# Kernel tuning notes

Hardware: AMD Instinct MI355X
Metric: run time of the kernel (lower is better)

Reference implementation:

```python
import jax, jax.numpy as jnp
import numpy as np

N, D, H, F, T = 2048, 256, 4, 64, 64
HF = H * F


def setup_inputs() -> dict:
    key = jax.random.key(0)
    ks = jax.random.split(key, 24)
    f32 = jnp.float32
    emb = jax.random.normal(ks[0], (N, D), f32)
    y_as_x = jax.random.normal(ks[1], (N, T), f32)
    adj = (jax.random.uniform(ks[2], (N, N)) < 0.02).astype(f32)
    u = lambda k, shape, s: jax.random.uniform(k, shape, f32, -s, s)
    stdv = 1.0 / np.sqrt(HF)
    inp = dict(emb=emb, y_as_x=y_as_x, adj=adj)
    for i, p in enumerate(['pos', 'neg']):
        o = 3 + i * 6
        inp[p + '_w'] = u(ks[o], (D, HF), stdv)
        inp[p + '_wu'] = u(ks[o + 1], (H, F), 1.0)
        inp[p + '_wv'] = u(ks[o + 2], (H, F), 1.0)
        inp[p + '_b'] = u(ks[o + 3], (1, HF), stdv)
        inp[p + '_pw'] = u(ks[o + 4], (D, HF), 0.02)
        inp[p + '_pb'] = jnp.zeros((HF,), f32)
    inp['self_w'] = u(ks[15], (D, D), 0.02)
    inp['self_b'] = jnp.zeros((D,), f32)
    inp['mlp_pos_w'] = u(ks[16], (HF, D), 0.02)
    inp['mlp_pos_b'] = jnp.zeros((D,), f32)
    inp['mlp_neg_w'] = u(ks[17], (HF, D), 0.02)
    inp['mlp_neg_b'] = jnp.zeros((D,), f32)
    inp['sem_w1'] = u(ks[18], (D, D), 0.02)
    inp['sem_b1'] = jnp.zeros((D,), f32)
    inp['sem_w2'] = u(ks[19], (D, 1), 0.02)
    return inp


def _gat(x, mask, w, wu, wv, b, pw, pb):
    # x: [N,D], mask: [N,N] bool; multi-head GAT with dense masked softmax
    s = (x @ w).reshape(N, H, F).transpose(1, 0, 2)          # [H,N,F]
    f1 = jnp.einsum('hnf,hf->hn', s, wu)                     # u-score per node
    f2 = jnp.einsum('hnf,hf->hn', s, wv)                     # v-score per node
    logits = f1[:, None, :] + f2[:, :, None]                 # [H,N,N], i<-j
    logits = jax.nn.leaky_relu(logits, 0.2)
    masked = jnp.where(mask[None], logits, -1e9)
    attn = jnp.where(mask[None], jax.nn.softmax(masked, axis=2), 0.0)
    out = jnp.einsum('hij,hjf->hif', attn, s)                # [H,N,F]
    out = out.transpose(1, 0, 2).reshape(N, HF) + b
    return out + x @ pw + pb


def reference(emb, y_as_x, adj, pos_w, pos_wu, pos_wv, pos_b, pos_pw, pos_pb,
              neg_w, neg_wu, neg_wv, neg_b, neg_pw, neg_pb,
              self_w, self_b, mlp_pos_w, mlp_pos_b, mlp_neg_w, mlp_neg_b,
              sem_w1, sem_b1, sem_w2):
    # batched pairwise correlation (replaces the per-node Python loop)
    yc = y_as_x - y_as_x.mean(axis=1, keepdims=True)         # centered
    dot = yc @ yc.T                                          # [N,N]
    std = jnp.sqrt((yc ** 2).sum(axis=1) / (T - 1))          # torch std: ddof=1
    corr = dot / (std[:, None] * std[None, :])
    edge = adj != 0
    pos_mask = edge & (corr >= 0.1)
    neg_mask = edge & (corr < 0.1)

    pos_sup = _gat(emb, pos_mask, pos_w, pos_wu, pos_wv, pos_b, pos_pw, pos_pb)
    neg_sup = _gat(emb, neg_mask, neg_w, neg_wu, neg_wv, neg_b, neg_pw, neg_pb)

    sup = emb @ self_w + self_b
    pos_sup = pos_sup @ mlp_pos_w + mlp_pos_b
    neg_sup = neg_sup @ mlp_neg_w + mlp_neg_b

    all_emb = jnp.stack((sup, pos_sup, neg_sup), axis=1)     # [N,3,D]
    # semantic attention over the 3 relation channels
    wlog = jnp.tanh(all_emb @ sem_w1 + sem_b1) @ sem_w2      # [N,3,1]
    beta = jax.nn.softmax(wlog, axis=1)
    x = (beta * all_emb).sum(axis=1)                         # [N,D]
    # PairNorm PN-SI
    x = x - x.mean(axis=0)
    rownorm = jnp.sqrt(1e-6 + (x ** 2).sum(axis=1, keepdims=True))
    return x / rownorm
```

## Files before the change

### kernel.cpp

```cpp
#include <hip/hip_runtime.h>
#include <hip/hip_bf16.h>

#define KN  2048
#define KD  256
#define KH  4
#define KF  64
#define KT  64
#define NCS 32

typedef __attribute__((ext_vector_type(8))) short short8;
typedef __attribute__((ext_vector_type(4))) float floatx4;

__device__ __forceinline__ float wave_sum(float v) {
    #pragma unroll
    for (int o = 32; o > 0; o >>= 1) v += __shfl_xor(v, o, 64);
    return v;
}
__device__ __forceinline__ float wave_max(float v) {
    #pragma unroll
    for (int o = 32; o > 0; o >>= 1) v = fmaxf(v, __shfl_xor(v, o, 64));
    return v;
}
__device__ __forceinline__ short f2bs(float x) {
    union { __hip_bfloat16 h; short s; } u;
    u.h = __float2bfloat16(x);
    return u.s;
}

__global__ __launch_bounds__(256) void setup_kernel(const float* __restrict__ y,
                                                    float* __restrict__ ycs) {
    int w = threadIdx.x >> 6, lane = threadIdx.x & 63;
    int n = blockIdx.x * 4 + w;
    float v = y[n * KT + lane];
    float mean = wave_sum(v) * (1.0f / KT);
    float yc = v - mean;
    float ss = wave_sum(yc * yc);
    ycs[n * KT + lane] = yc * rsqrtf(ss * (1.0f / (KT - 1)));
}

__device__ __forceinline__ void corr_body(const float* __restrict__ ycs,
                                          const float* __restrict__ adj,
                                          unsigned char* __restrict__ code,
                                          int blk, char* smem) {
    float (*As)[68] = (float(*)[68])smem;
    float (*Bs)[68] = (float(*)[68])(smem + 4352);
    int bi = 0, rem = blk;
    while (rem >= 32 - bi) { rem -= 32 - bi; bi++; }
    int bj = bi + rem;
    int i0 = bi * 64, j0 = bj * 64;
    int t = threadIdx.x;
    int tx = t & 15, ty = t >> 4;
    int ar = t >> 2, ac = (t & 3) * 4;
    float acc[4][4] = {};
    for (int kt = 0; kt < KT; kt += 16) {
        float4 a4 = *reinterpret_cast<const float4*>(&ycs[(size_t)(i0 + ar) * KT + kt + ac]);
        float4 b4 = *reinterpret_cast<const float4*>(&ycs[(size_t)(j0 + ar) * KT + kt + ac]);
        As[ac + 0][ar] = a4.x; As[ac + 1][ar] = a4.y; As[ac + 2][ar] = a4.z; As[ac + 3][ar] = a4.w;
        Bs[ac + 0][ar] = b4.x; Bs[ac + 1][ar] = b4.y; Bs[ac + 2][ar] = b4.z; Bs[ac + 3][ar] = b4.w;
        __syncthreads();
        #pragma unroll
        for (int kk = 0; kk < 16; kk++) {
            float4 av = *reinterpret_cast<const float4*>(&As[kk][ty * 4]);
            float4 bv = *reinterpret_cast<const float4*>(&Bs[kk][tx * 4]);
            float a4v[4] = {av.x, av.y, av.z, av.w};
            float b4v[4] = {bv.x, bv.y, bv.z, bv.w};
            #pragma unroll
            for (int ii = 0; ii < 4; ii++)
                #pragma unroll
                for (int jj = 0; jj < 4; jj++) acc[ii][jj] += a4v[ii] * b4v[jj];
        }
        __syncthreads();
    }
    #pragma unroll
    for (int ii = 0; ii < 4; ii++) {
        int i = i0 + ty * 4 + ii;
        int jb = j0 + tx * 4;
        float4 av4 = *reinterpret_cast<const float4*>(&adj[(size_t)i * KN + jb]);
        float a4v[4] = {av4.x, av4.y, av4.z, av4.w};
        uchar4 cc;
        unsigned char* c = (unsigned char*)&cc;
        #pragma unroll
        for (int jj = 0; jj < 4; jj++)
            c[jj] = (a4v[jj] != 0.0f) ? ((acc[ii][jj] >= 0.1f) ? 1 : 2) : 0;
        *reinterpret_cast<uchar4*>(&code[(size_t)i * KN + jb]) = cc;
    }
    if (bi != bj) {
        #pragma unroll
        for (int jj = 0; jj < 4; jj++) {
            int j = j0 + tx * 4 + jj;
            int ib = i0 + ty * 4;
            float4 av4 = *reinterpret_cast<const float4*>(&adj[(size_t)j * KN + ib]);
            float a4v[4] = {av4.x, av4.y, av4.z, av4.w};
            uchar4 cc;
            unsigned char* c = (unsigned char*)&cc;
            #pragma unroll
            for (int ii = 0; ii < 4; ii++)
                c[ii] = (a4v[ii] != 0.0f) ? ((acc[ii][jj] >= 0.1f) ? 1 : 2) : 0;
            *reinterpret_cast<uchar4*>(&code[(size_t)j * KN + ib]) = cc;
        }
    }
}

template <bool TANH>
__device__ __forceinline__ void mfma_gemm_body(
    const float* __restrict__ A, int lda, int bm,
    const float* __restrict__ B, int ldb, int bn,
    const float* __restrict__ bias,
    float* __restrict__ C, int ldc, int cn,
    float* __restrict__ f1h, float* __restrict__ f2h,
    const float* __restrict__ wu_h, const float* __restrict__ wv_h,
    char* smem)
{
    short* As = (short*)smem;
    short* Bs = (short*)(smem + 5120);
    int t = threadIdx.x;
    int w = t >> 6, lane = t & 63;
    int m16 = lane & 15, kq = lane >> 4;
    floatx4 acc0 = {0,0,0,0}, acc1 = {0,0,0,0}, acc2 = {0,0,0,0}, acc3 = {0,0,0,0};
    int ar = t >> 2, acq = (t & 3) * 8;
    int bnn = t & 63, bkg = (t >> 6) * 8;
    for (int kt = 0; kt < KD; kt += 32) {
        const float* pa = &A[(size_t)(bm + ar) * lda + kt + acq];
        float4 a0 = *(const float4*)pa;
        float4 a1 = *(const float4*)(pa + 4);
        short8 av;
        av[0] = f2bs(a0.x); av[1] = f2bs(a0.y); av[2] = f2bs(a0.z); av[3] = f2bs(a0.w);
        av[4] = f2bs(a1.x); av[5] = f2bs(a1.y); av[6] = f2bs(a1.z); av[7] = f2bs(a1.w);
        const float* pb = &B[(size_t)(kt + bkg) * ldb + bn + bnn];
        short8 bv;
        #pragma unroll
        for (int u = 0; u < 8; u++) bv[u] = f2bs(pb[(size_t)u * ldb]);
        __syncthreads();
        *(short8*)&As[ar * 40 + acq] = av;
        *(short8*)&Bs[bnn * 40 + bkg] = bv;
        __syncthreads();
        short8 af  = *(short8*)&As[(w * 16 + m16) * 40 + kq * 8];
        short8 bf0 = *(short8*)&Bs[( 0 + m16) * 40 + kq * 8];
        short8 bf1 = *(short8*)&Bs[(16 + m16) * 40 + kq * 8];
        short8 bf2 = *(short8*)&Bs[(32 + m16) * 40 + kq * 8];
        short8 bf3 = *(short8*)&Bs[(48 + m16) * 40 + kq * 8];
        acc0 = __builtin_amdgcn_mfma_f32_16x16x32_bf16(af, bf0, acc0, 0, 0, 0);
        acc1 = __builtin_amdgcn_mfma_f32_16x16x32_bf16(af, bf1, acc1, 0, 0, 0);
        acc2 = __builtin_amdgcn_mfma_f32_16x16x32_bf16(af, bf2, acc2, 0, 0, 0);
        acc3 = __builtin_amdgcn_mfma_f32_16x16x32_bf16(af, bf3, acc3, 0, 0, 0);
    }
    int row0 = bm + w * 16 + kq * 4;
    floatx4 accs[4] = {acc0, acc1, acc2, acc3};
    #pragma unroll
    for (int nb = 0; nb < 4; nb++) {
        #pragma unroll
        for (int r = 0; r < 4; r++) {
            int col = nb * 16 + m16;
            float v = accs[nb][r] + (bias ? bias[col] : 0.0f);
            if (TANH) {
                float vc = fminf(fmaxf(v, -9.0f), 9.0f);
                float ex = __expf(2.0f * vc);
                v = (ex - 1.0f) / (ex + 1.0f);
            }
            C[(size_t)(row0 + r) * ldc + cn + col] = v;
        }
    }
    if (f1h) {
        float wuv[4], wvv[4];
        #pragma unroll
        for (int nb = 0; nb < 4; nb++) { wuv[nb] = wu_h[nb * 16 + m16]; wvv[nb] = wv_h[nb * 16 + m16]; }
        #pragma unroll
        for (int r = 0; r < 4; r++) {
            float p1 = accs[0][r] * wuv[0] + accs[1][r] * wuv[1] + accs[2][r] * wuv[2] + accs[3][r] * wuv[3];
            float p2 = accs[0][r] * wvv[0] + accs[1][r] * wvv[1] + accs[2][r] * wvv[2] + accs[3][r] * wvv[3];
            #pragma unroll
            for (int o = 1; o < 16; o <<= 1) {
                p1 += __shfl_xor(p1, o, 64);
                p2 += __shfl_xor(p2, o, 64);
            }
            if (m16 == 0) { f1h[row0 + r] = p1; f2h[row0 + r] = p2; }
        }
    }
}

struct EmbPtrs {
    float *S_pos, *S_neg, *P_pos, *P_neg, *sup;
    float *f1p, *f2p, *f1n, *f2n;
};
__global__ __launch_bounds__(256, 4) void phase1_kernel(
    const float* __restrict__ ycs, const float* __restrict__ adj,
    unsigned char* __restrict__ code,
    const float* __restrict__ emb,
    const float* __restrict__ pos_w, const float* __restrict__ neg_w,
    const float* __restrict__ pos_pw, const float* __restrict__ neg_pw,
    const float* __restrict__ self_w,
    const float* __restrict__ pos_pb, const float* __restrict__ neg_pb,
    const float* __restrict__ self_b,
    const float* __restrict__ pos_wu, const float* __restrict__ pos_wv,
    const float* __restrict__ neg_wu, const float* __restrict__ neg_wv,
    float* __restrict__ colsum, EmbPtrs ep)
{
    __shared__ alignas(16) char smem[10240];
    int blk = blockIdx.x;
    if (blk < 528) {
        corr_body(ycs, adj, code, blk, smem);
        return;
    }
    if (blk >= 1168) {
        for (int j = threadIdx.x; j < NCS * KD; j += 256) colsum[j] = 0.0f;
        return;
    }
    int b = blk - 528;
    int tn = b % 20, tm = b / 20;
    int buf = tn >> 2, coloff = (tn & 3) * 64;
    int h = tn & 3;
    const float* B; const float* bias; float* C;
    float *f1h = nullptr, *f2h = nullptr;
    const float *wu_h = nullptr, *wv_h = nullptr;
    if (buf == 0) {
        B = pos_w;  bias = nullptr; C = ep.S_pos;
        f1h = ep.f1p + h * KN; f2h = ep.f2p + h * KN;
        wu_h = pos_wu + h * KF; wv_h = pos_wv + h * KF;
    } else if (buf == 1) {
        B = neg_w;  bias = nullptr; C = ep.S_neg;
        f1h = ep.f1n + h * KN; f2h = ep.f2n + h * KN;
        wu_h = neg_wu + h * KF; wv_h = neg_wv + h * KF;
    } else if (buf == 2) { B = pos_pw; bias = pos_pb + coloff;  C = ep.P_pos; }
    else if (buf == 3)   { B = neg_pw; bias = neg_pb + coloff;  C = ep.P_neg; }
    else                 { B = self_w; bias = self_b + coloff;  C = ep.sup; }
    mfma_gemm_body<false>(emb, KD, tm * 64, B, KD, coloff, bias,
                          C, KD, coloff, f1h, f2h, wu_h, wv_h, smem);
}

__global__ __launch_bounds__(256, 4) void gemm_mlp(const float* __restrict__ Astack,
                                                   const float* __restrict__ B0,
                                                   const float* __restrict__ B1,
                                                   const float* __restrict__ b0,
                                                   const float* __restrict__ b1,
                                                   float* __restrict__ Cstack,
                                                   const float* __restrict__ sup,
                                                   const float* __restrict__ semw1,
                                                   const float* __restrict__ semb1,
                                                   float* __restrict__ T0) {
    __shared__ alignas(16) char smem[10240];
    int by = blockIdx.y;
    int cn = blockIdx.x * 64;
    if (by < 64) {
        int bm = by * 64;
        bool sel = bm >= KN;
        mfma_gemm_body<false>(Astack, KD, bm, sel ? B1 : B0, KD, cn,
                              (sel ? b1 : b0) + cn, Cstack, KD, cn,
                              nullptr, nullptr, nullptr, nullptr, smem);
    } else {
        int bm = (by - 64) * 64;
        mfma_gemm_body<true>(sup, KD, bm, semw1, KD, cn,
                             semb1 + cn, T0, KD, cn,
                             nullptr, nullptr, nullptr, nullptr, smem);
    }
}

__global__ __launch_bounds__(256, 4) void gemm_sem(const float* __restrict__ Astack,
                                                   const float* __restrict__ B,
                                                   const float* __restrict__ bias,
                                                   float* __restrict__ Cstack) {
    __shared__ alignas(16) char smem[10240];
    int cn = blockIdx.x * 64;
    mfma_gemm_body<true>(Astack, KD, blockIdx.y * 64, B, KD, cn,
                         bias + cn, Cstack, KD, cn,
                         nullptr, nullptr, nullptr, nullptr, smem);
}

#define MAXE 256
__global__ __launch_bounds__(256) void attn_kernel(
    const unsigned char* __restrict__ code,
    const float* __restrict__ f1p, const float* __restrict__ f2p,
    const float* __restrict__ Sp, const float* __restrict__ Pp,
    const float* __restrict__ bp, float* __restrict__ Gp,
    const float* __restrict__ f1n, const float* __restrict__ f2n,
    const float* __restrict__ Sn, const float* __restrict__ Pn,
    const float* __restrict__ bn_, float* __restrict__ Gn)
{
    __shared__ alignas(16) int jlp[MAXE];
    __shared__ alignas(16) int jln[MAXE];
    __shared__ alignas(16) float lg[2][KH][MAXE];
    __shared__ int cntp, cntn;
    int i = blockIdx.x;
    int w = threadIdx.x >> 6, lane = threadIdx.x & 63;
    if (threadIdx.x == 0) { cntp = 0; cntn = 0; }
    __syncthreads();
    unsigned long long lmask = (1ull << lane) - 1ull;
    #pragma unroll
    for (int it = 0; it < 2; it++) {
        int base = w * 512 + it * 256;
        uchar4 cv = *reinterpret_cast<const uchar4*>(&code[(size_t)i * KN + base + lane * 4]);
        const unsigned char* ce = (const unsigned char*)&cv;
        #pragma unroll
        for (int e = 0; e < 4; e++) {
            bool ip = (ce[e] == (unsigned char)1);
            bool in_ = (ce[e] == (unsigned char)2);
            unsigned long long balp = __ballot(ip);
            unsigned long long baln = __ballot(in_);
            int tp = __popcll(balp), tn = __popcll(baln);
            int basep = 0, basen = 0;
            if (lane == 0) {
                if (tp) basep = atomicAdd(&cntp, tp);
                if (tn) basen = atomicAdd(&cntn, tn);
            }
            basep = __shfl(basep, 0, 64);
            basen = __shfl(basen, 0, 64);
            int j = base + lane * 4 + e;
            if (ip) { int idx = basep + __popcll(balp & lmask); if (idx < MAXE) jlp[idx] = j; }
            if (in_) { int idx = basen + __popcll(baln & lmask); if (idx < MAXE) jln[idx] = j; }
        }
    }
    __syncthreads();
    int cp = cntp; if (cp > MAXE) cp = MAXE;
    int cn2 = cntn; if (cn2 > MAXE) cn2 = MAXE;
    int cpR = (cp + 3) & ~3, cnR = (cn2 + 3) & ~3;
    if (threadIdx.x < cpR - cp) jlp[cp + threadIdx.x] = 0;
    if (threadIdx.x < cnR - cn2) jln[cn2 + threadIdx.x] = 0;
    __syncthreads();
    int h = w;
    int g = lane >> 4, q4 = (lane & 15) * 4;
    #pragma unroll
    for (int rel = 0; rel < 2; rel++) {
        const int* jl = rel ? jln : jlp;
        int count = rel ? cn2 : cp;
        int countR = rel ? cnR : cpR;
        const float* f1 = rel ? f1n : f1p;
        const float* f2 = rel ? f2n : f2p;
        const float* S  = rel ? Sn : Sp;
        const float* P  = rel ? Pn : Pp;
        const float* b  = rel ? bn_ : bp;
        float* G        = rel ? Gn : Gp;
        float* lgr = lg[rel][h];
        float f2i = f2[h * KN + i];
        float m = -1e30f;
        for (int k = lane; k < count; k += 64) {
            float x = f1[h * KN + jl[k]] + f2i;
            x = (x > 0.0f) ? x : 0.2f * x;
            lgr[k] = x;
            m = fmaxf(m, x);
        }
        m = wave_max(m);
        float ps = 0.0f;
        for (int k = lane; k < count; k += 64) {
            float e = __expf(lgr[k] - m);
            lgr[k] = e;
            ps += e;
        }
        float denom = wave_sum(ps);
        for (int k2 = count + lane; k2 < countR; k2 += 64) lgr[k2] = 0.0f;
        const float* Sh4 = S + h * KF + q4;
        float ax = 0.0f, ay = 0.0f, az = 0.0f, aw = 0.0f;
        for (int k = 0; k < countR; k += 4) {
            int j = jl[k + g];
            float wgt = lgr[k + g];
            float4 sv = *reinterpret_cast<const float4*>(&Sh4[(size_t)j * KD]);
            ax += wgt * sv.x; ay += wgt * sv.y; az += wgt * sv.z; aw += wgt * sv.w;
        }
        #pragma unroll
        for (int o = 16; o < 64; o <<= 1) {
            ax += __shfl_xor(ax, o, 64); ay += __shfl_xor(ay, o, 64);
            az += __shfl_xor(az, o, 64); aw += __shfl_xor(aw, o, 64);
        }
        if (g == 0) {
            float inv = count ? (1.0f / denom) : 0.0f;
            int col = h * KF + q4;
            size_t idx = (size_t)i * KD + col;
            float4 pv = *reinterpret_cast<const float4*>(&P[idx]);
            float4 o4;
            o4.x = ax * inv + b[col + 0] + pv.x;
            o4.y = ay * inv + b[col + 1] + pv.y;
            o4.z = az * inv + b[col + 2] + pv.z;
            o4.w = aw * inv + b[col + 3] + pv.w;
            *reinterpret_cast<float4*>(&G[idx]) = o4;
        }
    }
}

__global__ __launch_bounds__(256) void combine_kernel(const float* __restrict__ T0,
                                                      const float* __restrict__ T1,
                                                      const float* __restrict__ T2,
                                                      const float* __restrict__ w2,
                                                      const float* __restrict__ sup,
                                                      const float* __restrict__ psup,
                                                      const float* __restrict__ nsup,
                                                      float* __restrict__ X,
                                                      float* __restrict__ colsum) {
    int n = blockIdx.x, d = threadIdx.x;
    size_t idx = (size_t)n * KD + d;
    float w2d = w2[d];
    float p0 = T0[idx] * w2d, p1 = T1[idx] * w2d, p2 = T2[idx] * w2d;
    __shared__ float sbuf[4][3];
    int wv = d >> 6, lane = d & 63;
    float s0 = wave_sum(p0), s1 = wave_sum(p1), s2 = wave_sum(p2);
    if (lane == 0) { sbuf[wv][0] = s0; sbuf[wv][1] = s1; sbuf[wv][2] = s2; }
    __syncthreads();
    float w0 = sbuf[0][0] + sbuf[1][0] + sbuf[2][0] + sbuf[3][0];
    float w1 = sbuf[0][1] + sbuf[1][1] + sbuf[2][1] + sbuf[3][1];
    float w2l = sbuf[0][2] + sbuf[1][2] + sbuf[2][2] + sbuf[3][2];
    float mm = fmaxf(w0, fmaxf(w1, w2l));
    float e0 = __expf(w0 - mm), e1 = __expf(w1 - mm), e2 = __expf(w2l - mm);
    float inv = 1.0f / (e0 + e1 + e2);
    float x = (e0 * inv) * sup[idx] + (e1 * inv) * psup[idx] + (e2 * inv) * nsup[idx];
    X[idx] = x;
    atomicAdd(&colsum[(n & (NCS - 1)) * KD + d], x);
}

__global__ __launch_bounds__(256) void final_kernel(const float* __restrict__ X,
                                                    const float* __restrict__ colsum,
                                                    float* __restrict__ out) {
    int n = blockIdx.x, d = threadIdx.x;
    float cs = 0.0f;
    #pragma unroll
    for (int r = 0; r < NCS; r++) cs += colsum[r * KD + d];
    float mean = cs * (1.0f / KN);
    float xc = X[(size_t)n * KD + d] - mean;
    __shared__ float sbuf[4];
    int wv = d >> 6, lane = d & 63;
    float s = wave_sum(xc * xc);
    if (lane == 0) sbuf[wv] = s;
    __syncthreads();
    float ss = sbuf[0] + sbuf[1] + sbuf[2] + sbuf[3];
    out[(size_t)n * KD + d] = xc * rsqrtf(1e-6f + ss);
}

extern "C" void kernel_launch(void* const* d_in, const int* in_sizes, int n_in,
                              void* d_out, int out_size, void* d_ws, size_t ws_size,
                              hipStream_t stream) {
    typedef const float* fp;
    fp emb    = (fp)d_in[0];
    fp y_as_x = (fp)d_in[1];
    fp adj    = (fp)d_in[2];
    fp pos_w  = (fp)d_in[3],  pos_wu = (fp)d_in[4],  pos_wv = (fp)d_in[5];
    fp pos_b  = (fp)d_in[6],  pos_pw = (fp)d_in[7],  pos_pb = (fp)d_in[8];
    fp neg_w  = (fp)d_in[9],  neg_wu = (fp)d_in[10], neg_wv = (fp)d_in[11];
    fp neg_b  = (fp)d_in[12], neg_pw = (fp)d_in[13], neg_pb = (fp)d_in[14];
    fp self_w = (fp)d_in[15], self_b = (fp)d_in[16];
    fp mlp_pos_w = (fp)d_in[17], mlp_pos_b = (fp)d_in[18];
    fp mlp_neg_w = (fp)d_in[19], mlp_neg_b = (fp)d_in[20];
    fp sem_w1 = (fp)d_in[21], sem_b1 = (fp)d_in[22], sem_w2 = (fp)d_in[23];
    float* out = (float*)d_out;

    char* ws = (char*)d_ws;
    float* ycs        = (float*)(ws + 0x0000000);
    unsigned char* cd = (unsigned char*)(ws + 0x0080000);
    float* S_pos      = (float*)(ws + 0x0480000);
    float* S_neg      = (float*)(ws + 0x0680000);
    float* P_pos      = (float*)(ws + 0x0880000);
    float* P_neg      = (float*)(ws + 0x0A80000);
    float* G_pos      = (float*)(ws + 0x0C80000);
    float* G_neg      = (float*)(ws + 0x0E80000);
    float* sup        = (float*)(ws + 0x1080000);
    float* psup       = (float*)(ws + 0x1280000);
    float* nsup       = (float*)(ws + 0x1480000);
    float* colsum     = (float*)(ws + 0x1680000);
    float* f1p        = (float*)(ws + 0x1700000);
    float* f2p        = (float*)(ws + 0x1708000);
    float* f1n        = (float*)(ws + 0x1710000);
    float* f2n        = (float*)(ws + 0x1718000);
    float* T0 = P_pos, *T1 = P_neg, *T2 = G_pos, *X = G_neg;

    setup_kernel<<<512, 256, 0, stream>>>(y_as_x, ycs);

    EmbPtrs ep = {S_pos, S_neg, P_pos, P_neg, sup, f1p, f2p, f1n, f2n};
    phase1_kernel<<<528 + 640 + 1, 256, 0, stream>>>(ycs, adj, cd, emb,
                                                     pos_w, neg_w, pos_pw, neg_pw, self_w,
                                                     pos_pb, neg_pb, self_b,
                                                     pos_wu, pos_wv, neg_wu, neg_wv,
                                                     colsum, ep);

    attn_kernel<<<KN, 256, 0, stream>>>(cd,
                                        f1p, f2p, S_pos, P_pos, pos_b, G_pos,
                                        f1n, f2n, S_neg, P_neg, neg_b, G_neg);

    gemm_mlp<<<dim3(4, 96), 256, 0, stream>>>(G_pos, mlp_pos_w, mlp_neg_w,
                                              mlp_pos_b, mlp_neg_b, psup,
                                              sup, sem_w1, sem_b1, T0);
    gemm_sem<<<dim3(4, 64), 256, 0, stream>>>(psup, sem_w1, sem_b1, T1);

    combine_kernel<<<KN, 256, 0, stream>>>(T0, T1, T2, sem_w2, sup, psup, nsup, X, colsum);
    final_kernel<<<KN, 256, 0, stream>>>(X, colsum, out);
}
```

Before: 171.7 us.

## Fuse all stages into one persistent kernel with software grid barriers

Replaces the seven separate kernel launches with a single persistent mega-kernel of 768 blocks. Each former kernel becomes a grid-stride loop over virtual blocks, and stages are separated by atomic-counter grid barriers. The barrier counters are zeroed by a memset before launch. The aim is to remove launch and inter-kernel drain gaps, at the cost of spin-wait barriers, a requirement that all 768 blocks be co-resident, and lower parallelism in stages that previously used more blocks.

After: 648.2 us. +277.6%, slower.

```diff
diff --git a/kernel.cpp b/kernel.cpp
--- a/kernel.cpp
+++ b/kernel.cpp
@@ -7,6 +7,8 @@
 #define KF  64
 #define KT  64
 #define NCS 32
+#define MAXE 256
+#define NBLK 768
 
 typedef __attribute__((ext_vector_type(8))) short short8;
 typedef __attribute__((ext_vector_type(4))) float floatx4;
@@ -27,16 +29,33 @@
     return u.s;
 }
 
-__global__ __launch_bounds__(256) void setup_kernel(const float* __restrict__ y,
-                                                    float* __restrict__ ycs) {
-    int w = threadIdx.x >> 6, lane = threadIdx.x & 63;
-    int n = blockIdx.x * 4 + w;
-    float v = y[n * KT + lane];
-    float mean = wave_sum(v) * (1.0f / KT);
-    float yc = v - mean;
-    float ss = wave_sum(yc * yc);
-    ycs[n * KT + lane] = yc * rsqrtf(ss * (1.0f / (KT - 1)));
-}
+__device__ __forceinline__ void soft_sync(unsigned* bar, int idx) {
+    __syncthreads();
+    if (threadIdx.x == 0) {
+        __threadfence();
+        atomicAdd(&bar[idx], 1u);
+        while (atomicAdd(&bar[idx], 0u) < (unsigned)NBLK)
+            __builtin_amdgcn_s_sleep(8);
+        __threadfence();
+    }
+    __syncthreads();
+}
+
+struct MegaArgs {
+    const float *y, *adj, *emb;
+    const float *pos_w, *neg_w, *pos_pw, *neg_pw, *self_w;
+    const float *pos_pb, *neg_pb, *self_b;
+    const float *pos_wu, *pos_wv, *neg_wu, *neg_wv;
+    const float *pos_b, *neg_b;
+    const float *mlp_pos_w, *mlp_pos_b, *mlp_neg_w, *mlp_neg_b;
+    const float *sem_w1, *sem_b1, *sem_w2;
+    float *ycs; unsigned char *cd;
+    float *S_pos, *S_neg, *P_pos, *P_neg, *sup, *psup, *nsup;
+    float *G_pos, *G_neg, *T0, *T1, *T2, *X, *colsum;
+    float *f1p, *f2p, *f1n, *f2n;
+    unsigned *bar;
+    float *out;
+};
 
 __device__ __forceinline__ void corr_body(const float* __restrict__ ycs,
                                           const float* __restrict__ adj,
@@ -178,116 +197,19 @@
     }
 }
 
-struct EmbPtrs {
-    float *S_pos, *S_neg, *P_pos, *P_neg, *sup;
-    float *f1p, *f2p, *f1n, *f2n;
-};
-__global__ __launch_bounds__(256, 4) void phase1_kernel(
-    const float* __restrict__ ycs, const float* __restrict__ adj,
-    unsigned char* __restrict__ code,
-    const float* __restrict__ emb,
-    const float* __restrict__ pos_w, const float* __restrict__ neg_w,
-    const float* __restrict__ pos_pw, const float* __restrict__ neg_pw,
-    const float* __restrict__ self_w,
-    const float* __restrict__ pos_pb, const float* __restrict__ neg_pb,
-    const float* __restrict__ self_b,
-    const float* __restrict__ pos_wu, const float* __restrict__ pos_wv,
-    const float* __restrict__ neg_wu, const float* __restrict__ neg_wv,
-    float* __restrict__ colsum, EmbPtrs ep)
-{
-    __shared__ alignas(16) char smem[10240];
-    int blk = blockIdx.x;
-    if (blk < 528) {
-        corr_body(ycs, adj, code, blk, smem);
-        return;
-    }
-    if (blk >= 1168) {
-        for (int j = threadIdx.x; j < NCS * KD; j += 256) colsum[j] = 0.0f;
-        return;
-    }
-    int b = blk - 528;
-    int tn = b % 20, tm = b / 20;
-    int buf = tn >> 2, coloff = (tn & 3) * 64;
-    int h = tn & 3;
-    const float* B; const float* bias; float* C;
-    float *f1h = nullptr, *f2h = nullptr;
-    const float *wu_h = nullptr, *wv_h = nullptr;
-    if (buf == 0) {
-        B = pos_w;  bias = nullptr; C = ep.S_pos;
-        f1h = ep.f1p + h * KN; f2h = ep.f2p + h * KN;
-        wu_h = pos_wu + h * KF; wv_h = pos_wv + h * KF;
-    } else if (buf == 1) {
-        B = neg_w;  bias = nullptr; C = ep.S_neg;
-        f1h = ep.f1n + h * KN; f2h = ep.f2n + h * KN;
-        wu_h = neg_wu + h * KF; wv_h = neg_wv + h * KF;
-    } else if (buf == 2) { B = pos_pw; bias = pos_pb + coloff;  C = ep.P_pos; }
-    else if (buf == 3)   { B = neg_pw; bias = neg_pb + coloff;  C = ep.P_neg; }
-    else                 { B = self_w; bias = self_b + coloff;  C = ep.sup; }
-    mfma_gemm_body<false>(emb, KD, tm * 64, B, KD, coloff, bias,
-                          C, KD, coloff, f1h, f2h, wu_h, wv_h, smem);
-}
-
-__global__ __launch_bounds__(256, 4) void gemm_mlp(const float* __restrict__ Astack,
-                                                   const float* __restrict__ B0,
-                                                   const float* __restrict__ B1,
-                                                   const float* __restrict__ b0,
-                                                   const float* __restrict__ b1,
-                                                   float* __restrict__ Cstack,
-                                                   const float* __restrict__ sup,
-                                                   const float* __restrict__ semw1,
-                                                   const float* __restrict__ semb1,
-                                                   float* __restrict__ T0) {
-    __shared__ alignas(16) char smem[10240];
-    int by = blockIdx.y;
-    int cn = blockIdx.x * 64;
-    if (by < 64) {
-        int bm = by * 64;
-        bool sel = bm >= KN;
-        mfma_gemm_body<false>(Astack, KD, bm, sel ? B1 : B0, KD, cn,
-                              (sel ? b1 : b0) + cn, Cstack, KD, cn,
-                              nullptr, nullptr, nullptr, nullptr, smem);
-    } else {
-        int bm = (by - 64) * 64;
-        mfma_gemm_body<true>(sup, KD, bm, semw1, KD, cn,
-                             semb1 + cn, T0, KD, cn,
-                             nullptr, nullptr, nullptr, nullptr, smem);
-    }
-}
-
-__global__ __launch_bounds__(256, 4) void gemm_sem(const float* __restrict__ Astack,
-                                                   const float* __restrict__ B,
-                                                   const float* __restrict__ bias,
-                                                   float* __restrict__ Cstack) {
-    __shared__ alignas(16) char smem[10240];
-    int cn = blockIdx.x * 64;
-    mfma_gemm_body<true>(Astack, KD, blockIdx.y * 64, B, KD, cn,
-                         bias + cn, Cstack, KD, cn,
-                         nullptr, nullptr, nullptr, nullptr, smem);
-}
-
-#define MAXE 256
-__global__ __launch_bounds__(256) void attn_kernel(
-    const unsigned char* __restrict__ code,
-    const float* __restrict__ f1p, const float* __restrict__ f2p,
-    const float* __restrict__ Sp, const float* __restrict__ Pp,
-    const float* __restrict__ bp, float* __restrict__ Gp,
-    const float* __restrict__ f1n, const float* __restrict__ f2n,
-    const float* __restrict__ Sn, const float* __restrict__ Pn,
-    const float* __restrict__ bn_, float* __restrict__ Gn)
-{
-    __shared__ alignas(16) int jlp[MAXE];
-    __shared__ alignas(16) int jln[MAXE];
-    __shared__ alignas(16) float lg[2][KH][MAXE];
-    __shared__ int cntp, cntn;
-    int i = blockIdx.x;
+__device__ __forceinline__ void attn_body(const MegaArgs& a, int i, char* smem) {
+    int* jlp = (int*)smem;
+    int* jln = (int*)(smem + 1024);
+    float* lg = (float*)(smem + 2048);
+    int* cnts = (int*)(smem + 10240);
     int w = threadIdx.x >> 6, lane = threadIdx.x & 63;
-    if (threadIdx.x == 0) { cntp = 0; cntn = 0; }
+    if (threadIdx.x == 0) { cnts[0] = 0; cnts[1] = 0; }
     __syncthreads();
     unsigned long long lmask = (1ull << lane) - 1ull;
     #pragma unroll
     for (int it = 0; it < 2; it++) {
         int base = w * 512 + it * 256;
-        uchar4 cv = *reinterpret_cast<const uchar4*>(&code[(size_t)i * KN + base + lane * 4]);
+        uchar4 cv = *reinterpret_cast<const uchar4*>(&a.cd[(size_t)i * KN + base + lane * 4]);
         const unsigned char* ce = (const unsigned char*)&cv;
         #pragma unroll
         for (int e = 0; e < 4; e++) {
@@ -298,8 +220,8 @@
             int tp = __popcll(balp), tn = __popcll(baln);
             int basep = 0, basen = 0;
             if (lane == 0) {
-                if (tp) basep = atomicAdd(&cntp, tp);
-                if (tn) basen = atomicAdd(&cntn, tn);
+                if (tp) basep = atomicAdd(&cnts[0], tp);
+                if (tn) basen = atomicAdd(&cnts[1], tn);
             }
             basep = __shfl(basep, 0, 64);
             basen = __shfl(basen, 0, 64);
@@ -309,8 +231,8 @@
         }
     }
     __syncthreads();
-    int cp = cntp; if (cp > MAXE) cp = MAXE;
-    int cn2 = cntn; if (cn2 > MAXE) cn2 = MAXE;
+    int cp = cnts[0]; if (cp > MAXE) cp = MAXE;
+    int cn2 = cnts[1]; if (cn2 > MAXE) cn2 = MAXE;
     int cpR = (cp + 3) & ~3, cnR = (cn2 + 3) & ~3;
     if (threadIdx.x < cpR - cp) jlp[cp + threadIdx.x] = 0;
     if (threadIdx.x < cnR - cn2) jln[cn2 + threadIdx.x] = 0;
@@ -322,13 +244,13 @@
         const int* jl = rel ? jln : jlp;
         int count = rel ? cn2 : cp;
         int countR = rel ? cnR : cpR;
-        const float* f1 = rel ? f1n : f1p;
-        const float* f2 = rel ? f2n : f2p;
-        const float* S  = rel ? Sn : Sp;
-        const float* P  = rel ? Pn : Pp;
-        const float* b  = rel ? bn_ : bp;
-        float* G        = rel ? Gn : Gp;
-        float* lgr = lg[rel][h];
+        const float* f1 = rel ? a.f1n : a.f1p;
+        const float* f2 = rel ? a.f2n : a.f2p;
+        const float* S  = rel ? a.S_neg : a.S_pos;
+        const float* P  = rel ? a.P_neg : a.P_pos;
+        const float* b  = rel ? a.neg_b : a.pos_b;
+        float* G        = rel ? a.G_neg : a.G_pos;
+        float* lgr = lg + (rel * KH + h) * MAXE;
         float f2i = f2[h * KN + i];
         float m = -1e30f;
         for (int k = lane; k < count; k += 64) {
@@ -374,107 +296,170 @@
     }
 }
 
-__global__ __launch_bounds__(256) void combine_kernel(const float* __restrict__ T0,
-                                                      const float* __restrict__ T1,
-                                                      const float* __restrict__ T2,
-                                                      const float* __restrict__ w2,
-                                                      const float* __restrict__ sup,
-                                                      const float* __restrict__ psup,
-                                                      const float* __restrict__ nsup,
-                                                      float* __restrict__ X,
-                                                      float* __restrict__ colsum) {
-    int n = blockIdx.x, d = threadIdx.x;
+__device__ __forceinline__ void combine_body(const MegaArgs& a, int n, char* smem) {
+    float* sbuf = (float*)smem;
+    int d = threadIdx.x;
     size_t idx = (size_t)n * KD + d;
-    float w2d = w2[d];
-    float p0 = T0[idx] * w2d, p1 = T1[idx] * w2d, p2 = T2[idx] * w2d;
-    __shared__ float sbuf[4][3];
+    float w2d = a.sem_w2[d];
+    float p0 = a.T0[idx] * w2d, p1 = a.T1[idx] * w2d, p2 = a.T2[idx] * w2d;
     int wv = d >> 6, lane = d & 63;
     float s0 = wave_sum(p0), s1 = wave_sum(p1), s2 = wave_sum(p2);
-    if (lane == 0) { sbuf[wv][0] = s0; sbuf[wv][1] = s1; sbuf[wv][2] = s2; }
-    __syncthreads();
-    float w0 = sbuf[0][0] + sbuf[1][0] + sbuf[2][0] + sbuf[3][0];
-    float w1 = sbuf[0][1] + sbuf[1][1] + sbuf[2][1] + sbuf[3][1];
-    float w2l = sbuf[0][2] + sbuf[1][2] + sbuf[2][2] + sbuf[3][2];
+    if (lane == 0) { sbuf[wv * 3 + 0] = s0; sbuf[wv * 3 + 1] = s1; sbuf[wv * 3 + 2] = s2; }
+    __syncthreads();
+    float w0 = sbuf[0] + sbuf[3] + sbuf[6] + sbuf[9];
+    float w1 = sbuf[1] + sbuf[4] + sbuf[7] + sbuf[10];
+    float w2l = sbuf[2] + sbuf[5] + sbuf[8] + sbuf[11];
     float mm = fmaxf(w0, fmaxf(w1, w2l));
     float e0 = __expf(w0 - mm), e1 = __expf(w1 - mm), e2 = __expf(w2l - mm);
     float inv = 1.0f / (e0 + e1 + e2);
-    float x = (e0 * inv) * sup[idx] + (e1 * inv) * psup[idx] + (e2 * inv) * nsup[idx];
-    X[idx] = x;
-    atomicAdd(&colsum[(n & (NCS - 1)) * KD + d], x);
-}
-
-__global__ __launch_bounds__(256) void final_kernel(const float* __restrict__ X,
-                                                    const float* __restrict__ colsum,
-                                                    float* __restrict__ out) {
-    int n = blockIdx.x, d = threadIdx.x;
+    float x = (e0 * inv) * a.sup[idx] + (e1 * inv) * a.psup[idx] + (e2 * inv) * a.nsup[idx];
+    a.X[idx] = x;
+    atomicAdd(&a.colsum[(n & (NCS - 1)) * KD + d], x);
+    __syncthreads();
+}
+
+__device__ __forceinline__ void final_body(const MegaArgs& a, int n, char* smem) {
+    float* sbuf = (float*)smem;
+    int d = threadIdx.x;
     float cs = 0.0f;
     #pragma unroll
-    for (int r = 0; r < NCS; r++) cs += colsum[r * KD + d];
+    for (int r = 0; r < NCS; r++) cs += a.colsum[r * KD + d];
     float mean = cs * (1.0f / KN);
-    float xc = X[(size_t)n * KD + d] - mean;
-    __shared__ float sbuf[4];
+    float xc = a.X[(size_t)n * KD + d] - mean;
     int wv = d >> 6, lane = d & 63;
     float s = wave_sum(xc * xc);
     if (lane == 0) sbuf[wv] = s;
     __syncthreads();
     float ss = sbuf[0] + sbuf[1] + sbuf[2] + sbuf[3];
-    out[(size_t)n * KD + d] = xc * rsqrtf(1e-6f + ss);
+    a.out[(size_t)n * KD + d] = xc * rsqrtf(1e-6f + ss);
+    __syncthreads();
+}
+
+__global__ __launch_bounds__(256, 4) void mega_kernel(MegaArgs a) {
+    __shared__ alignas(16) char smem[10368];
+    const int nb = NBLK;
+
+    for (int vb = blockIdx.x; vb < 513; vb += nb) {
+        if (vb < 512) {
+            int w = threadIdx.x >> 6, lane = threadIdx.x & 63;
+            int n = vb * 4 + w;
+            float v = a.y[n * KT + lane];
+            float mean = wave_sum(v) * (1.0f / KT);
+            float yc = v - mean;
+            float ss = wave_sum(yc * yc);
+            a.ycs[n * KT + lane] = yc * rsqrtf(ss * (1.0f / (KT - 1)));
+        } else {
+            for (int j = threadIdx.x; j < NCS * KD; j += 256) a.colsum[j] = 0.0f;
+        }
+    }
+    soft_sync(a.bar, 0);
+
+    for (int vb = blockIdx.x; vb < 1168; vb += nb) {
+        if (vb < 528) {
+            corr_body(a.ycs, a.adj, a.cd, vb, smem);
+        } else {
+            int b = vb - 528;
+            int tn = b % 20, tm = b / 20;
+            int buf = tn >> 2, coloff = (tn & 3) * 64;
+            int h = tn & 3;
+            const float* B; const float* bias; float* C;
+            float *f1h = nullptr, *f2h = nullptr;
+            const float *wu_h = nullptr, *wv_h = nullptr;
+            if (buf == 0) {
+                B = a.pos_w;  bias = nullptr; C = a.S_pos;
+                f1h = a.f1p + h * KN; f2h = a.f2p + h * KN;
+                wu_h = a.pos_wu + h * KF; wv_h = a.pos_wv + h * KF;
+            } else if (buf == 1) {
+                B = a.neg_w;  bias = nullptr; C = a.S_neg;
+                f1h = a.f1n + h * KN; f2h = a.f2n + h * KN;
+                wu_h = a.neg_wu + h * KF; wv_h = a.neg_wv + h * KF;
+            } else if (buf == 2) { B = a.pos_pw; bias = a.pos_pb + coloff; C = a.P_pos; }
+            else if (buf == 3)   { B = a.neg_pw; bias = a.neg_pb + coloff; C = a.P_neg; }
+            else                 { B = a.self_w; bias = a.self_b + coloff; C = a.sup; }
+            mfma_gemm_body<false>(a.emb, KD, tm * 64, B, KD, coloff, bias,
+                                  C, KD, coloff, f1h, f2h, wu_h, wv_h, smem);
+        }
+        __syncthreads();
+    }
+    soft_sync(a.bar, 1);
+
+    for (int vb = blockIdx.x; vb < 2048; vb += nb) {
+        attn_body(a, vb, smem);
+        __syncthreads();
+    }
+    soft_sync(a.bar, 2);
+
+    for (int vb = blockIdx.x; vb < 384; vb += nb) {
+        int bx = vb & 3, by = vb >> 2;
+        int cn = bx * 64;
+        if (by < 64) {
+            int bm = by * 64;
+            bool sel = bm >= KN;
+            mfma_gemm_body<false>(a.G_pos, KD, bm, sel ? a.mlp_neg_w : a.mlp_pos_w, KD, cn,
+                                  (sel ? a.mlp_neg_b : a.mlp_pos_b) + cn, a.psup, KD, cn,
+                                  nullptr, nullptr, nullptr, nullptr, smem);
+        } else {
+            int bm = (by - 64) * 64;
+            mfma_gemm_body<true>(a.sup, KD, bm, a.sem_w1, KD, cn,
+                                 a.sem_b1 + cn, a.T0, KD, cn,
+                                 nullptr, nullptr, nullptr, nullptr, smem);
+        }
+    }
+    soft_sync(a.bar, 3);
+
+    for (int vb = blockIdx.x; vb < 256; vb += nb) {
+        int bx = vb & 3, by = vb >> 2;
+        int cn = bx * 64;
+        mfma_gemm_body<true>(a.psup, KD, by * 64, a.sem_w1, KD, cn,
+                             a.sem_b1 + cn, a.T1, KD, cn,
+                             nullptr, nullptr, nullptr, nullptr, smem);
+    }
+    soft_sync(a.bar, 4);
+
+    for (int vb = blockIdx.x; vb < 2048; vb += nb) combine_body(a, vb, smem);
+    soft_sync(a.bar, 5);
+
+    for (int vb = blockIdx.x; vb < 2048; vb += nb) final_body(a, vb, smem);
 }
 
 extern "C" void kernel_launch(void* const* d_in, const int* in_sizes, int n_in,
                               void* d_out, int out_size, void* d_ws, size_t ws_size,
                               hipStream_t stream) {
     typedef const float* fp;
-    fp emb    = (fp)d_in[0];
-    fp y_as_x = (fp)d_in[1];
-    fp adj    = (fp)d_in[2];
-    fp pos_w  = (fp)d_in[3],  pos_wu = (fp)d_in[4],  pos_wv = (fp)d_in[5];
-    fp pos_b  = (fp)d_in[6],  pos_pw = (fp)d_in[7],  pos_pb = (fp)d_in[8];
-    fp neg_w  = (fp)d_in[9],  neg_wu = (fp)d_in[10], neg_wv = (fp)d_in[11];
-    fp neg_b  = (fp)d_in[12], neg_pw = (fp)d_in[13], neg_pb = (fp)d_in[14];
-    fp self_w = (fp)d_in[15], self_b = (fp)d_in[16];
-    fp mlp_pos_w = (fp)d_in[17], mlp_pos_b = (fp)d_in[18];
-    fp mlp_neg_w = (fp)d_in[19], mlp_neg_b = (fp)d_in[20];
-    fp sem_w1 = (fp)d_in[21], sem_b1 = (fp)d_in[22], sem_w2 = (fp)d_in[23];
-    float* out = (float*)d_out;
+    MegaArgs a;
+    a.emb    = (fp)d_in[0];
+    a.y      = (fp)d_in[1];
+    a.adj    = (fp)d_in[2];
+    a.pos_w  = (fp)d_in[3];  a.pos_wu = (fp)d_in[4];  a.pos_wv = (fp)d_in[5];
+    a.pos_b  = (fp)d_in[6];  a.pos_pw = (fp)d_in[7];  a.pos_pb = (fp)d_in[8];
+    a.neg_w  = (fp)d_in[9];  a.neg_wu = (fp)d_in[10]; a.neg_wv = (fp)d_in[11];
+    a.neg_b  = (fp)d_in[12]; a.neg_pw = (fp)d_in[13]; a.neg_pb = (fp)d_in[14];
+    a.self_w = (fp)d_in[15]; a.self_b = (fp)d_in[16];
+    a.mlp_pos_w = (fp)d_in[17]; a.mlp_pos_b = (fp)d_in[18];
+    a.mlp_neg_w = (fp)d_in[19]; a.mlp_neg_b = (fp)d_in[20];
+    a.sem_w1 = (fp)d_in[21]; a.sem_b1 = (fp)d_in[22]; a.sem_w2 = (fp)d_in[23];
+    a.out = (float*)d_out;
 
     char* ws = (char*)d_ws;
-    float* ycs        = (float*)(ws + 0x0000000);
-    unsigned char* cd = (unsigned char*)(ws + 0x0080000);
-    float* S_pos      = (float*)(ws + 0x0480000);
-    float* S_neg      = (float*)(ws + 0x0680000);
-    float* P_pos      = (float*)(ws + 0x0880000);
-    float* P_neg      = (float*)(ws + 0x0A80000);
-    float* G_pos      = (float*)(ws + 0x0C80000);
-    float* G_neg      = (float*)(ws + 0x0E80000);
-    float* sup        = (float*)(ws + 0x1080000);
-    float* psup       = (float*)(ws + 0x1280000);
-    float* nsup       = (float*)(ws + 0x1480000);
-    float* colsum     = (float*)(ws + 0x1680000);
-    float* f1p        = (float*)(ws + 0x1700000);
-    float* f2p        = (float*)(ws + 0x1708000);
-    float* f1n        = (float*)(ws + 0x1710000);
-    float* f2n        = (float*)(ws + 0x1718000);
-    float* T0 = P_pos, *T1 = P_neg, *T2 = G_pos, *X = G_neg;
-
-    setup_kernel<<<512, 256, 0, stream>>>(y_as_x, ycs);
-
-    EmbPtrs ep = {S_pos, S_neg, P_pos, P_neg, sup, f1p, f2p, f1n, f2n};
-    phase1_kernel<<<528 + 640 + 1, 256, 0, stream>>>(ycs, adj, cd, emb,
-                                                     pos_w, neg_w, pos_pw, neg_pw, self_w,
-                                                     pos_pb, neg_pb, self_b,
-                                                     pos_wu, pos_wv, neg_wu, neg_wv,
-                                                     colsum, ep);
-
-    attn_kernel<<<KN, 256, 0, stream>>>(cd,
-                                        f1p, f2p, S_pos, P_pos, pos_b, G_pos,
-                                        f1n, f2n, S_neg, P_neg, neg_b, G_neg);
-
-    gemm_mlp<<<dim3(4, 96), 256, 0, stream>>>(G_pos, mlp_pos_w, mlp_neg_w,
-                                              mlp_pos_b, mlp_neg_b, psup,
-                                              sup, sem_w1, sem_b1, T0);
-    gemm_sem<<<dim3(4, 64), 256, 0, stream>>>(psup, sem_w1, sem_b1, T1);
-
-    combine_kernel<<<KN, 256, 0, stream>>>(T0, T1, T2, sem_w2, sup, psup, nsup, X, colsum);
-    final_kernel<<<KN, 256, 0, stream>>>(X, colsum, out);
-}
+    a.ycs    = (float*)(ws + 0x0000000);
+    a.cd     = (unsigned char*)(ws + 0x0080000);
+    a.S_pos  = (float*)(ws + 0x0480000);
+    a.S_neg  = (float*)(ws + 0x0680000);
+    a.P_pos  = (float*)(ws + 0x0880000);
+    a.P_neg  = (float*)(ws + 0x0A80000);
+    a.G_pos  = (float*)(ws + 0x0C80000);
+    a.G_neg  = (float*)(ws + 0x0E80000);
+    a.sup    = (float*)(ws + 0x1080000);
+    a.psup   = (float*)(ws + 0x1280000);
+    a.nsup   = (float*)(ws + 0x1480000);
+    a.colsum = (float*)(ws + 0x1680000);
+    a.f1p    = (float*)(ws + 0x1700000);
+    a.f2p    = (float*)(ws + 0x1708000);
+    a.f1n    = (float*)(ws + 0x1710000);
+    a.f2n    = (float*)(ws + 0x1718000);
+    a.bar    = (unsigned*)(ws + 0x1720000);
+    a.T0 = a.P_pos; a.T1 = a.P_neg; a.T2 = a.G_pos; a.X = a.G_neg;
+
+    hipMemsetAsync(a.bar, 0, 64, stream);
+    mega_kernel<<<NBLK, 256, 0, stream>>>(a);
+}
```
